# Optimization experiments

Measured on AMD Instinct MI355X. Metric: run time of the kernel, lower is better.

The kernel has to match this reference:

```python
import jax, jax.numpy as jnp
import numpy as np

N_NODES = 100000
N_EDGES = 1600000
D = 64        # atom_embed_dim
EF = 4        # edge_feat_dim
V = 100       # num_elements


def setup_inputs() -> dict:
    key = jax.random.key(0)
    ks = jax.random.split(key, 10)
    x_ids = jax.random.randint(ks[0], (N_NODES,), 0, V, dtype=jnp.int64 if jax.config.jax_enable_x64 else jnp.int32)
    edge_index = jax.random.randint(ks[1], (2, N_EDGES), 0, N_NODES, dtype=jnp.int64 if jax.config.jax_enable_x64 else jnp.int32)
    edge_attr = jax.random.normal(ks[2], (N_EDGES, EF), dtype=jnp.float32)
    emb = jax.random.normal(ks[3], (V, D), dtype=jnp.float32)
    s_in = 1.0 / np.sqrt(D + EF)
    s_d = 1.0 / np.sqrt(D)
    W1 = jax.random.uniform(ks[4], (D, D + EF), jnp.float32, -s_in, s_in)
    b1 = jax.random.uniform(ks[5], (D,), jnp.float32, -s_in, s_in)
    Wu1 = jax.random.uniform(ks[6], (D, D), jnp.float32, -s_d, s_d)
    bu1 = jax.random.uniform(ks[7], (D,), jnp.float32, -s_d, s_d)
    W2 = jax.random.uniform(ks[8], (D, D + EF), jnp.float32, -s_in, s_in)
    b2 = jax.random.uniform(ks[9], (D,), jnp.float32, -s_in, s_in)
    k2 = jax.random.split(jax.random.key(1), 2)
    Wu2 = jax.random.uniform(k2[0], (D, D), jnp.float32, -s_d, s_d)
    bu2 = jax.random.uniform(k2[1], (D,), jnp.float32, -s_d, s_d)
    return {"x_ids": x_ids, "edge_index": edge_index, "edge_attr": edge_attr,
            "emb": emb, "W1": W1, "b1": b1, "Wu1": Wu1, "bu1": bu1,
            "W2": W2, "b2": b2, "Wu2": Wu2, "bu2": bu2}


def _round(x, src, dst, edge_attr, Wm, bm, Wu, bu):
    # gather src node feats, concat edge feats, msg MLP, scatter-add to dst
    m = jnp.concatenate([x[src], edge_attr], axis=-1)       # (E, D+EF)
    m = jax.nn.relu(m @ Wm.T + bm)                           # (E, D)
    agg = jax.ops.segment_sum(m, dst, num_segments=x.shape[0])  # (N, D)
    return jax.nn.relu((x + agg) @ Wu.T + bu)                # (N, D)


def reference(x_ids, edge_index, edge_attr, emb, W1, b1, Wu1, bu1, W2, b2, Wu2, bu2):
    src, dst = edge_index[0], edge_index[1]
    x = emb[x_ids]                                           # (N, D)
    x = _round(x, src, dst, edge_attr, W1, b1, Wu1, bu1)
    x = _round(x, src, dst, edge_attr, W2, b2, Wu2, bu2)
    return x.mean(axis=0)                                    # (D,)
```

## Files before the change

kernel.cpp:

```cpp
#include <hip/hip_runtime.h>

#define DD    64
#define WCOLS 68
#define VV    100

__device__ __forceinline__ float lane_bcast(float v, int k) {
    return __int_as_float(__builtin_amdgcn_readlane(__float_as_int(v), k));
}

__global__ __launch_bounds__(256) void hist_kernel(
    const int* __restrict__ dst, int* __restrict__ deg, int E)
{
    int i = blockIdx.x * 256 + threadIdx.x;
    int stride = gridDim.x * 256;
    for (; i < E; i += stride) atomicAdd(&deg[dst[i]], 1);
}

__global__ __launch_bounds__(256) void scan1_kernel(
    const int* __restrict__ deg, int* __restrict__ rowp, int* __restrict__ bsum, int N)
{
    __shared__ int lds[256];
    int base = blockIdx.x * 1024;
    int t = threadIdx.x;
    int idx0 = base + t * 4;
    int v[4];
    #pragma unroll
    for (int j = 0; j < 4; ++j) v[j] = (idx0 + j < N) ? deg[idx0 + j] : 0;
    lds[t] = v[0] + v[1] + v[2] + v[3];
    __syncthreads();
    for (int off = 1; off < 256; off <<= 1) {
        int x = (t >= off) ? lds[t - off] : 0;
        __syncthreads();
        lds[t] += x;
        __syncthreads();
    }
    int run = (t > 0) ? lds[t - 1] : 0;
    if (t == 255) bsum[blockIdx.x] = lds[255];
    #pragma unroll
    for (int j = 0; j < 4; ++j) {
        if (idx0 + j < N) rowp[idx0 + j] = run;
        run += v[j];
    }
}

__global__ __launch_bounds__(256) void scan2_kernel(int* __restrict__ bsum, int nchunks)
{
    __shared__ int lds[256];
    int t = threadIdx.x;
    int v = (t < nchunks) ? bsum[t] : 0;
    lds[t] = v;
    __syncthreads();
    for (int off = 1; off < 256; off <<= 1) {
        int x = (t >= off) ? lds[t - off] : 0;
        __syncthreads();
        lds[t] += x;
        __syncthreads();
    }
    if (t < nchunks) bsum[t] = (t > 0) ? lds[t - 1] : 0;
}

__global__ __launch_bounds__(256) void scan3_kernel(
    int* __restrict__ rowp, const int* __restrict__ bsum, int* __restrict__ cursor,
    int N, int E)
{
    int i = blockIdx.x * 256 + threadIdx.x;
    if (i == 0) rowp[N] = E;
    if (i < N) {
        int v = rowp[i] + bsum[i >> 10];
        rowp[i] = v;
        cursor[i] = v;
    }
}

__global__ __launch_bounds__(256) void fill_kernel(
    const int* __restrict__ src, const int* __restrict__ dst,
    const int* __restrict__ x_ids, const float* __restrict__ eattr,
    int* __restrict__ cursor,
    int* __restrict__ srcp, unsigned char* __restrict__ vb,
    float4* __restrict__ eap, int E)
{
    int i = blockIdx.x * 256 + threadIdx.x;
    int stride = gridDim.x * 256;
    for (; i < E; i += stride) {
        int s = src[i];
        int d = dst[i];
        int pos = atomicAdd(&cursor[d], 1);
        srcp[pos] = s;
        vb[pos]   = (unsigned char)x_ids[s];
        eap[pos]  = *(const float4*)(eattr + (size_t)i * 4);
    }
}

__global__ __launch_bounds__(256) void vocab_kernel(
    const float* __restrict__ emb, const float* __restrict__ W1,
    const float* __restrict__ b1, float* __restrict__ YV)
{
    __shared__ float WaT[64 * 64];
    for (int i = threadIdx.x; i < 64 * 64; i += 256) {
        int d = i & 63, k = i >> 6;
        WaT[i] = W1[d * WCOLS + k];
    }
    __syncthreads();

    int lane = threadIdx.x & 63;
    int wv = blockIdx.x * 4 + (threadIdx.x >> 6);
    if (wv >= VV) return;
    float xv = emb[wv * DD + lane];
    float acc = b1[lane];
    #pragma unroll 8
    for (int k = 0; k < 64; ++k)
        acc = fmaf(WaT[k * 64 + lane], lane_bcast(xv, k), acc);
    YV[wv * DD + lane] = acc;
}

__global__ __launch_bounds__(256) void round1_kernel(
    const int* __restrict__ rowp, const unsigned char* __restrict__ vb,
    const float4* __restrict__ eap, const float* __restrict__ YV,
    const int* __restrict__ x_ids, const float* __restrict__ emb,
    const float* __restrict__ W1,
    const float* __restrict__ Wu, const float* __restrict__ bu,
    const float* __restrict__ Wn, const float* __restrict__ bn,
    float* __restrict__ x1, float* __restrict__ Yb, int N)
{
    __shared__ float YVs[VV * 64];
    __shared__ float WuT[64 * 64];
    __shared__ float WnT[64 * 64];
    for (int i = threadIdx.x; i < VV * 64; i += 256) YVs[i] = YV[i];
    for (int i = threadIdx.x; i < 64 * 64; i += 256) {
        int d = i & 63, k = i >> 6;
        WuT[i] = Wu[d * DD + k];
        WnT[i] = Wn[d * WCOLS + k];
    }
    __syncthreads();

    int lane = threadIdx.x & 63;
    int wid  = __builtin_amdgcn_readfirstlane((blockIdx.x * 256 + (int)threadIdx.x) >> 6);
    int nw   = (gridDim.x * 256) >> 6;
    float w0 = W1[lane * WCOLS + 64];
    float w1 = W1[lane * WCOLS + 65];
    float w2 = W1[lane * WCOLS + 66];
    float w3 = W1[lane * WCOLS + 67];
    float biasu = bu[lane];
    float biasn = bn[lane];

    for (int n = wid; n < N; n += nw) {
        int beg = rowp[n], end = rowp[n + 1];
        float acc = 0.f;
        int e = beg;
        for (; e + 3 < end; e += 4) {
            int v0 = vb[e], v1 = vb[e + 1], v2 = vb[e + 2], v3 = vb[e + 3];
            float4 a0 = eap[e], a1 = eap[e + 1], a2 = eap[e + 2], a3 = eap[e + 3];
            float y0 = YVs[v0 * 64 + lane];
            float y1 = YVs[v1 * 64 + lane];
            float y2 = YVs[v2 * 64 + lane];
            float y3 = YVs[v3 * 64 + lane];
            float m0 = y0 + w0 * a0.x + w1 * a0.y + w2 * a0.z + w3 * a0.w;
            float m1 = y1 + w0 * a1.x + w1 * a1.y + w2 * a1.z + w3 * a1.w;
            float m2 = y2 + w0 * a2.x + w1 * a2.y + w2 * a2.z + w3 * a2.w;
            float m3 = y3 + w0 * a3.x + w1 * a3.y + w2 * a3.z + w3 * a3.w;
            acc += fmaxf(m0, 0.f) + fmaxf(m1, 0.f) + fmaxf(m2, 0.f) + fmaxf(m3, 0.f);
        }
        for (; e < end; ++e) {
            int v0 = vb[e];
            float4 a0 = eap[e];
            float y0 = YVs[v0 * 64 + lane];
            float m0 = y0 + w0 * a0.x + w1 * a0.y + w2 * a0.z + w3 * a0.w;
            acc += fmaxf(m0, 0.f);
        }

        int id = x_ids[n];
        float v = emb[(size_t)id * DD + lane] + acc;
        float au = biasu;
        #pragma unroll 8
        for (int k = 0; k < 64; ++k)
            au = fmaf(WuT[k * 64 + lane], lane_bcast(v, k), au);
        float oo = fmaxf(au, 0.f);

        float an = biasn;
        #pragma unroll 8
        for (int k = 0; k < 64; ++k)
            an = fmaf(WnT[k * 64 + lane], lane_bcast(oo, k), an);

        size_t o = (size_t)n * DD + lane;
        x1[o] = oo;
        Yb[o] = an;
    }
}

__global__ __launch_bounds__(256) void round2_kernel(
    const int* __restrict__ rowp, const int* __restrict__ srcp,
    const float4* __restrict__ eap, const float* __restrict__ Y_in,
    const float* __restrict__ Wm,
    const float* __restrict__ Wu, const float* __restrict__ bu,
    const float* __restrict__ x1, float* __restrict__ out_mean,
    int N, float inv_n)
{
    __shared__ float WuT[64 * 64];
    __shared__ float red[256];
    for (int i = threadIdx.x; i < 64 * 64; i += 256) {
        int d = i & 63, k = i >> 6;
        WuT[i] = Wu[d * DD + k];
    }
    __syncthreads();

    int lane = threadIdx.x & 63;
    int wid  = __builtin_amdgcn_readfirstlane((blockIdx.x * 256 + (int)threadIdx.x) >> 6);
    int nw   = (gridDim.x * 256) >> 6;
    float w0 = Wm[lane * WCOLS + 64];
    float w1 = Wm[lane * WCOLS + 65];
    float w2 = Wm[lane * WCOLS + 66];
    float w3 = Wm[lane * WCOLS + 67];
    float biasu = bu[lane];
    float lsum = 0.f;

    for (int n = wid; n < N; n += nw) {
        int beg = rowp[n], end = rowp[n + 1];
        float acc = 0.f;
        int e = beg;
        for (; e + 3 < end; e += 4) {
            int s0 = srcp[e], s1 = srcp[e + 1], s2 = srcp[e + 2], s3 = srcp[e + 3];
            float4 a0 = eap[e], a1 = eap[e + 1], a2 = eap[e + 2], a3 = eap[e + 3];
            float y0 = Y_in[(size_t)s0 * DD + lane];
            float y1 = Y_in[(size_t)s1 * DD + lane];
            float y2 = Y_in[(size_t)s2 * DD + lane];
            float y3 = Y_in[(size_t)s3 * DD + lane];
            float m0 = y0 + w0 * a0.x + w1 * a0.y + w2 * a0.z + w3 * a0.w;
            float m1 = y1 + w0 * a1.x + w1 * a1.y + w2 * a1.z + w3 * a1.w;
            float m2 = y2 + w0 * a2.x + w1 * a2.y + w2 * a2.z + w3 * a2.w;
            float m3 = y3 + w0 * a3.x + w1 * a3.y + w2 * a3.z + w3 * a3.w;
            acc += fmaxf(m0, 0.f) + fmaxf(m1, 0.f) + fmaxf(m2, 0.f) + fmaxf(m3, 0.f);
        }
        for (; e < end; ++e) {
            int s0 = srcp[e];
            float4 a0 = eap[e];
            float y0 = Y_in[(size_t)s0 * DD + lane];
            float m0 = y0 + w0 * a0.x + w1 * a0.y + w2 * a0.z + w3 * a0.w;
            acc += fmaxf(m0, 0.f);
        }

        size_t o = (size_t)n * DD + lane;
        float v = x1[o] + acc;
        float au = biasu;
        #pragma unroll 8
        for (int k = 0; k < 64; ++k)
            au = fmaf(WuT[k * 64 + lane], lane_bcast(v, k), au);
        lsum += fmaxf(au, 0.f);
    }

    red[threadIdx.x] = lsum;
    __syncthreads();
    if (threadIdx.x < 64) {
        float s = red[threadIdx.x] + red[threadIdx.x + 64] +
                  red[threadIdx.x + 128] + red[threadIdx.x + 192];
        unsafeAtomicAdd(&out_mean[threadIdx.x], s * inv_n);
    }
}

extern "C" void kernel_launch(void* const* d_in, const int* in_sizes, int n_in,
                              void* d_out, int out_size, void* d_ws, size_t ws_size,
                              hipStream_t stream) {
    const int*   x_ids = (const int*)d_in[0];
    const int*   ei    = (const int*)d_in[1];
    const float* eattr = (const float*)d_in[2];
    const float* emb   = (const float*)d_in[3];
    const float* W1    = (const float*)d_in[4];
    const float* b1    = (const float*)d_in[5];
    const float* Wu1   = (const float*)d_in[6];
    const float* bu1   = (const float*)d_in[7];
    const float* W2    = (const float*)d_in[8];
    const float* b2    = (const float*)d_in[9];
    const float* Wu2   = (const float*)d_in[10];
    const float* bu2   = (const float*)d_in[11];

    const int N = in_sizes[0];
    const int E = in_sizes[1] / 2;
    const int* src = ei;
    const int* dst = ei + E;

    float* ws = (float*)d_ws;
    size_t stride = (size_t)N * DD;
    float*  x1   = ws;
    float*  Yb   = ws + stride;
    float*  eapf = ws + 2 * stride;
    int*    srcp = (int*)(eapf + (size_t)E * 4);
    int*    rowp = srcp + E;
    int*    deg  = rowp + N + 1;
    int*    cur  = deg + N;
    int*    bsum = cur + N;
    float*  YV   = (float*)(bsum + 256);
    unsigned char* vb = (unsigned char*)(YV + VV * 64);
    float4* eap  = (float4*)eapf;

    float* out = (float*)d_out;
    float inv_n = 1.0f / (float)N;
    int nchunks = (N + 1023) / 1024;

    hipMemsetAsync(deg, 0, (size_t)N * sizeof(int), stream);
    hipMemsetAsync(out, 0, DD * sizeof(float), stream);

    hist_kernel <<<2048, 256, 0, stream>>>(dst, deg, E);
    scan1_kernel<<<nchunks, 256, 0, stream>>>(deg, rowp, bsum, N);
    scan2_kernel<<<1, 256, 0, stream>>>(bsum, nchunks);
    scan3_kernel<<<(N + 255) / 256, 256, 0, stream>>>(rowp, bsum, cur, N, E);
    fill_kernel <<<2048, 256, 0, stream>>>(src, dst, x_ids, eattr, cur, srcp, vb, eap, E);

    vocab_kernel<<<(VV + 3) / 4, 256, 0, stream>>>(emb, W1, b1, YV);

    round1_kernel<<<2048, 256, 0, stream>>>(
        rowp, vb, eap, YV, x_ids, emb, W1, Wu1, bu1, W2, b2, x1, Yb, N);
    round2_kernel<<<2048, 256, 0, stream>>>(
        rowp, srcp, eap, Yb, W2, Wu2, bu2, x1, out, N, inv_n);
}
```

Measured before the change: 607.2 us.

## Split round-2 node projection into separate kernel with 4-node register blocking

Moves the per-node Wn projection out of round1_kernel into a new yb_kernel that handles 4 nodes per wave, so each LDS weight read feeds 4 FMAs. This cuts round1's LDS footprint (one fewer 16KB weight table), which may raise occupancy. The edge loop in round1 is also unrolled to 8 with explicit fma chains. The cost is one extra launch plus writing x1 and reading it back from global memory.

```diff
diff --git a/kernel.cpp b/kernel.cpp
--- a/kernel.cpp
+++ b/kernel.cpp
@@ -119,17 +119,14 @@
     const int* __restrict__ x_ids, const float* __restrict__ emb,
     const float* __restrict__ W1,
     const float* __restrict__ Wu, const float* __restrict__ bu,
-    const float* __restrict__ Wn, const float* __restrict__ bn,
-    float* __restrict__ x1, float* __restrict__ Yb, int N)
+    float* __restrict__ x1, int N)
 {
     __shared__ float YVs[VV * 64];
     __shared__ float WuT[64 * 64];
-    __shared__ float WnT[64 * 64];
     for (int i = threadIdx.x; i < VV * 64; i += 256) YVs[i] = YV[i];
     for (int i = threadIdx.x; i < 64 * 64; i += 256) {
         int d = i & 63, k = i >> 6;
         WuT[i] = Wu[d * DD + k];
-        WnT[i] = Wn[d * WCOLS + k];
     }
     __syncthreads();
 
@@ -141,30 +138,34 @@
     float w2 = W1[lane * WCOLS + 66];
     float w3 = W1[lane * WCOLS + 67];
     float biasu = bu[lane];
-    float biasn = bn[lane];
 
     for (int n = wid; n < N; n += nw) {
         int beg = rowp[n], end = rowp[n + 1];
         float acc = 0.f;
         int e = beg;
-        for (; e + 3 < end; e += 4) {
-            int v0 = vb[e], v1 = vb[e + 1], v2 = vb[e + 2], v3 = vb[e + 3];
-            float4 a0 = eap[e], a1 = eap[e + 1], a2 = eap[e + 2], a3 = eap[e + 3];
-            float y0 = YVs[v0 * 64 + lane];
-            float y1 = YVs[v1 * 64 + lane];
-            float y2 = YVs[v2 * 64 + lane];
-            float y3 = YVs[v3 * 64 + lane];
-            float m0 = y0 + w0 * a0.x + w1 * a0.y + w2 * a0.z + w3 * a0.w;
-            float m1 = y1 + w0 * a1.x + w1 * a1.y + w2 * a1.z + w3 * a1.w;
-            float m2 = y2 + w0 * a2.x + w1 * a2.y + w2 * a2.z + w3 * a2.w;
-            float m3 = y3 + w0 * a3.x + w1 * a3.y + w2 * a3.z + w3 * a3.w;
-            acc += fmaxf(m0, 0.f) + fmaxf(m1, 0.f) + fmaxf(m2, 0.f) + fmaxf(m3, 0.f);
+        for (; e + 7 < end; e += 8) {
+            int   v8[8]; float4 a8[8];
+            #pragma unroll
+            for (int j = 0; j < 8; ++j) { v8[j] = vb[e + j]; a8[j] = eap[e + j]; }
+            float y8[8];
+            #pragma unroll
+            for (int j = 0; j < 8; ++j) y8[j] = YVs[v8[j] * 64 + lane];
+            #pragma unroll
+            for (int j = 0; j < 8; ++j) {
+                float m = fmaf(w0, a8[j].x, y8[j]);
+                m = fmaf(w1, a8[j].y, m);
+                m = fmaf(w2, a8[j].z, m);
+                m = fmaf(w3, a8[j].w, m);
+                acc += fmaxf(m, 0.f);
+            }
         }
         for (; e < end; ++e) {
             int v0 = vb[e];
             float4 a0 = eap[e];
-            float y0 = YVs[v0 * 64 + lane];
-            float m0 = y0 + w0 * a0.x + w1 * a0.y + w2 * a0.z + w3 * a0.w;
+            float m0 = fmaf(w0, a0.x, YVs[v0 * 64 + lane]);
+            m0 = fmaf(w1, a0.y, m0);
+            m0 = fmaf(w2, a0.z, m0);
+            m0 = fmaf(w3, a0.w, m0);
             acc += fmaxf(m0, 0.f);
         }
 
@@ -174,16 +175,44 @@
         #pragma unroll 8
         for (int k = 0; k < 64; ++k)
             au = fmaf(WuT[k * 64 + lane], lane_bcast(v, k), au);
-        float oo = fmaxf(au, 0.f);
-
-        float an = biasn;
+        x1[(size_t)n * DD + lane] = fmaxf(au, 0.f);
+    }
+}
+
+__global__ __launch_bounds__(256) void yb_kernel(
+    const float* __restrict__ x1, const float* __restrict__ Wn,
+    const float* __restrict__ bn, float* __restrict__ Yb, int N)
+{
+    __shared__ float WnT[64 * 64];
+    for (int i = threadIdx.x; i < 64 * 64; i += 256) {
+        int d = i & 63, k = i >> 6;
+        WnT[i] = Wn[d * WCOLS + k];
+    }
+    __syncthreads();
+
+    int lane = threadIdx.x & 63;
+    int wid  = (blockIdx.x * 256 + threadIdx.x) >> 6;
+    int nw   = (gridDim.x * 256) >> 6;
+    float bias = bn[lane];
+
+    for (int base = wid * 4; base < N; base += nw * 4) {
+        int nvalid = N - base; if (nvalid > 4) nvalid = 4;
+        float xv[4], acc[4];
+        #pragma unroll
+        for (int j = 0; j < 4; ++j) {
+            xv[j] = (j < nvalid) ? x1[(size_t)(base + j) * DD + lane] : 0.f;
+            acc[j] = bias;
+        }
         #pragma unroll 8
-        for (int k = 0; k < 64; ++k)
-            an = fmaf(WnT[k * 64 + lane], lane_bcast(oo, k), an);
-
-        size_t o = (size_t)n * DD + lane;
-        x1[o] = oo;
-        Yb[o] = an;
+        for (int k = 0; k < 64; ++k) {
+            float w = WnT[k * 64 + lane];
+            #pragma unroll
+            for (int j = 0; j < 4; ++j)
+                acc[j] = fmaf(w, lane_bcast(xv[j], k), acc[j]);
+        }
+        #pragma unroll
+        for (int j = 0; j < 4; ++j)
+            if (j < nvalid) Yb[(size_t)(base + j) * DD + lane] = acc[j];
     }
 }
 
@@ -307,7 +336,8 @@
     vocab_kernel<<<(VV + 3) / 4, 256, 0, stream>>>(emb, W1, b1, YV);
 
     round1_kernel<<<2048, 256, 0, stream>>>(
-        rowp, vb, eap, YV, x_ids, emb, W1, Wu1, bu1, W2, b2, x1, Yb, N);
+        rowp, vb, eap, YV, x_ids, emb, W1, Wu1, bu1, x1, N);
+    yb_kernel<<<1024, 256, 0, stream>>>(x1, W2, b2, Yb, N);
     round2_kernel<<<2048, 256, 0, stream>>>(
         rowp, srcp, eap, Yb, W2, Wu2, bu2, x1, out, N, inv_n);
 }
```

After: 596.9 us. No clear change (-1.7%).
